# Performance work log

Hardware: AMD Instinct MI355X
Metric: run time of the kernel (lower is better)

The kernel has to match this reference:

```python
import jax, jax.numpy as jnp
import numpy as np

NUM_PRIMARY_CAPS = 8
PRIMARY_DIM = 8
NUM_CLASSES = 10
OUT_DIM = 16
CHANNELS = 32
NUM_ROUTING = 3
IN_UNITS1 = CHANNELS * 20 * 20  # 12800


def squash(s):
    # squash as written in the source: |s| / (1 + |s|^2) * s
    n = jnp.linalg.norm(s, axis=-1, keepdims=True)
    return n / (1.0 + n * n) * s


def routing(u_hat, num_routing):
    # u_hat: [B, num_caps, in_units, dim_caps]
    b = jnp.zeros(u_hat.shape[:3] + (1,), dtype=u_hat.dtype)
    v = None
    for it in range(num_routing):
        c = jax.nn.softmax(b, axis=1)                       # over num_caps
        s = jnp.sum(c * u_hat, axis=2, keepdims=True)        # [B,J,1,M]
        v = squash(s)
        if it < num_routing - 1:
            b = b + jnp.sum(u_hat * v, axis=-1, keepdims=True)
    return v[:, :, 0, :]                                     # [B, num_caps, dim_caps]


def setup_inputs() -> dict:
    key = jax.random.key(0)
    k1, k2, k3, k4, k5 = jax.random.split(key, 5)
    x = jax.random.normal(k1, (64, 1, 28, 28), dtype=jnp.float32)
    conv_w = jax.random.normal(k2, (CHANNELS, 1, 9, 9), dtype=jnp.float32) * 0.05
    conv_b = jax.random.normal(k3, (CHANNELS,), dtype=jnp.float32) * 0.05
    # W: [num_capsules, in_units, dim_capsules, in_channels]
    W1 = jax.random.normal(k4, (NUM_PRIMARY_CAPS, IN_UNITS1, PRIMARY_DIM, CHANNELS), dtype=jnp.float32) * 0.05
    W2 = jax.random.normal(k5, (NUM_CLASSES, NUM_PRIMARY_CAPS, OUT_DIM, PRIMARY_DIM), dtype=jnp.float32) * 0.05
    return {"x": x, "conv_w": conv_w, "conv_b": conv_b, "W1": W1, "W2": W2}


def reference(x, conv_w, conv_b, W1, W2):
    B = x.shape[0]
    # conv1 + relu: [B,1,28,28] -> [B,C,20,20]
    h = jax.lax.conv_general_dilated(
        x, conv_w, window_strides=(1, 1), padding='VALID',
        dimension_numbers=('NCHW', 'OIHW', 'NCHW'))
    h = jax.nn.relu(h + conv_b[None, :, None, None])
    # primary capsules: flatten features to in_units; the source einsum
    # 'ijkl,ijkm->ijkm' reduces W over its in_channels axis and broadcasts x,
    # so u_hat[b,j,k,m] = sum_c W1[j,k,m,c] * x[b,k]
    xf = h.reshape(B, IN_UNITS1)
    u1 = jnp.einsum('jkmc,bk->bjkm', W1, xf)   # [B, 8, 12800, primary_dim]
    v1 = routing(u1, 1)                         # [B, 8, primary_dim]
    # digit capsules: per-unit feature vectors, standard capsule transform
    u2 = jnp.einsum('jkmc,bkc->bjkm', W2, v1)   # [B, 10, 8, out_dim]
    v2 = routing(u2, NUM_ROUTING)               # [B, 10, out_dim]
    return v2
```

## Files before the change

kernel.cpp:

```cpp
#include <hip/hip_runtime.h>

typedef float f4 __attribute__((ext_vector_type(4)));

__device__ __forceinline__ float readlane_f(float v, int l) {
    return __int_as_float(__builtin_amdgcn_readlane(__float_as_int(v), l));
}

__global__ __launch_bounds__(256) void conv_kernel(
    const float* __restrict__ X, const float* __restrict__ CW, const float* __restrict__ CB,
    float* __restrict__ XT, float* __restrict__ S1acc)
{
    int blk = blockIdx.x;
    int b = blk >> 5, c = blk & 31;
    int t = threadIdx.x;
    if (blk < 16) S1acc[blk * 256 + t] = 0.0f;

    __shared__ float xs[784];
    const f4* xb4 = reinterpret_cast<const f4*>(X + b * 784);
    if (t < 196) {
        f4 v = xb4[t];
        float* d = &xs[t * 4];
        d[0] = v.x; d[1] = v.y; d[2] = v.z; d[3] = v.w;
    }
    __syncthreads();

    float bias = CB[c];
    const float* wcg = CW + c * 81;
    float w[81];
    #pragma unroll
    for (int i = 0; i < 81; ++i) w[i] = wcg[i];

    for (int p = t; p < 400; p += 256) {
        int py = p / 20, px = p - py * 20;
        float acc = bias;
        #pragma unroll
        for (int dy = 0; dy < 9; ++dy) {
            const float* xr = &xs[(py + dy) * 28 + px];
            #pragma unroll
            for (int dx = 0; dx < 9; ++dx)
                acc = fmaf(xr[dx], w[dy * 9 + dx], acc);
        }
        XT[(size_t)(c * 400 + p) * 64 + b] = acc > 0.f ? acc : 0.f;
    }
}

__global__ __launch_bounds__(256) void primary_kernel(
    const float* __restrict__ W1, const float* __restrict__ XT, float* __restrict__ S1acc)
{
    int kb = blockIdx.x;
    int j  = blockIdx.y;
    int t = threadIdx.x;
    int wave = t >> 6, lane = t & 63;
    int k0 = kb * 64 + wave * 16;
    const f4* Wp = reinterpret_cast<const f4*>(W1) + (size_t)j * 819200
                   + (size_t)k0 * 64 + lane;
    const float* Xp = XT + (size_t)k0 * 64 + lane;

    float acc[8] = {0.f,0.f,0.f,0.f,0.f,0.f,0.f,0.f};
    #pragma unroll 8
    for (int kk = 0; kk < 16; ++kk) {
        f4 w = __builtin_nontemporal_load(Wp); Wp += 64;
        float xv = *Xp; Xp += 64;
        float s = (w.x + w.y) + (w.z + w.w);
        s += __shfl_xor(s, 1);
        s += __shfl_xor(s, 2);
        s += __shfl_xor(s, 4);
        #pragma unroll
        for (int m = 0; m < 8; ++m)
            acc[m] = fmaf(xv, readlane_f(s, m * 8), acc[m]);
    }

    __shared__ float red[4][64][9];
    #pragma unroll
    for (int m = 0; m < 8; ++m) red[wave][lane][m] = acc[m];
    __syncthreads();
    for (int idx = t; idx < 512; idx += 256) {
        int bb = idx >> 3, m = idx & 7;
        float v = red[0][bb][m] + red[1][bb][m] + red[2][bb][m] + red[3][bb][m];
        atomicAdd(&S1acc[(bb * 8 + j) * 8 + m], v);
    }
}

__global__ __launch_bounds__(256) void routing_kernel(
    const float* __restrict__ W2, const float* __restrict__ S1acc,
    float* __restrict__ OUT)
{
    int b = blockIdx.x;
    int t = threadIdx.x;
    __shared__ float v1[64];
    __shared__ float u2[10][8][16];
    __shared__ float blog[10][8];
    __shared__ float cw[10][8];
    __shared__ float sv[10][16];
    __shared__ float vv[10][16];
    __shared__ float fac[16];

    if (t < 64) v1[t] = S1acc[b * 64 + t] * 0.125f;
    if (t >= 64 && t < 144) { int q = t - 64; blog[q >> 3][q & 7] = 0.f; }
    __syncthreads();
    if (t < 8) {
        float n2 = 0.f;
        #pragma unroll
        for (int m = 0; m < 8; ++m) { float x = v1[t * 8 + m]; n2 = fmaf(x, x, n2); }
        float n = sqrtf(n2);
        fac[t] = n / (1.f + n2);
    }
    __syncthreads();
    if (t < 64) v1[t] *= fac[t >> 3];
    __syncthreads();

    for (int idx = t; idx < 1280; idx += 256) {
        int j = idx >> 7;
        int r = idx & 127;
        int k = r >> 4, m = r & 15;
        const float* wp = W2 + idx * 8;
        float a = 0.f;
        #pragma unroll
        for (int c = 0; c < 8; ++c) a = fmaf(wp[c], v1[k * 8 + c], a);
        u2[j][k][m] = a;
    }
    __syncthreads();

    for (int it = 0; it < 3; ++it) {
        if (t < 8) {
            float mx = -1e30f;
            #pragma unroll
            for (int j = 0; j < 10; ++j) mx = fmaxf(mx, blog[j][t]);
            float e[10], se = 0.f;
            #pragma unroll
            for (int j = 0; j < 10; ++j) { e[j] = expf(blog[j][t] - mx); se += e[j]; }
            float inv = 1.f / se;
            #pragma unroll
            for (int j = 0; j < 10; ++j) cw[j][t] = e[j] * inv;
        }
        __syncthreads();
        if (t < 160) {
            int j = t >> 4, m = t & 15;
            float a = 0.f;
            #pragma unroll
            for (int k = 0; k < 8; ++k) a = fmaf(cw[j][k], u2[j][k][m], a);
            sv[j][m] = a;
        }
        __syncthreads();
        if (t < 10) {
            float n2 = 0.f;
            #pragma unroll
            for (int m = 0; m < 16; ++m) { float x = sv[t][m]; n2 = fmaf(x, x, n2); }
            float n = sqrtf(n2);
            fac[t] = n / (1.f + n2);
        }
        __syncthreads();
        if (t < 160) { int j = t >> 4, m = t & 15; vv[j][m] = sv[j][m] * fac[j]; }
        __syncthreads();
        if (it < 2) {
            if (t < 80) {
                int j = t >> 3, k = t & 7;
                float d = 0.f;
                #pragma unroll
                for (int m = 0; m < 16; ++m) d = fmaf(u2[j][k][m], vv[j][m], d);
                blog[j][k] += d;
            }
            __syncthreads();
        }
    }
    if (t < 160) OUT[b * 160 + t] = vv[t >> 4][t & 15];
}

extern "C" void kernel_launch(void* const* d_in, const int* in_sizes, int n_in,
                              void* d_out, int out_size, void* d_ws, size_t ws_size,
                              hipStream_t stream) {
    const float* X  = (const float*)d_in[0];
    const float* CW = (const float*)d_in[1];
    const float* CB = (const float*)d_in[2];
    const float* W1 = (const float*)d_in[3];
    const float* W2 = (const float*)d_in[4];
    float* S1 = (float*)d_ws;
    float* XT = (float*)((char*)d_ws + 16384);
    float* OUT = (float*)d_out;

    conv_kernel<<<2048, 256, 0, stream>>>(X, CW, CB, XT, S1);
    primary_kernel<<<dim3(200, 8), 256, 0, stream>>>(W1, XT, S1);
    routing_kernel<<<64, 256, 0, stream>>>(W2, S1, OUT);
}
```

Before: 172.7 us.

## Batch conv across images per block for coalesced stores; enlarge primary blocks

The conv kernel now runs one block per (row-pair, channel) and handles all 64 images, so each thread owns one image and writes to the batch-innermost XT layout with coalesced stores instead of strided single-float writes. Input rows for all images are staged in padded shared memory (about 72KB), which may limit occupancy. The primary kernel doubles its block to 512 threads covering 128 input units, halving the number of atomic adds into the accumulator.

```diff
diff --git a/kernel.cpp b/kernel.cpp
--- a/kernel.cpp
+++ b/kernel.cpp
@@ -10,17 +10,26 @@
     const float* __restrict__ X, const float* __restrict__ CW, const float* __restrict__ CB,
     float* __restrict__ XT, float* __restrict__ S1acc)
 {
-    int blk = blockIdx.x;
-    int b = blk >> 5, c = blk & 31;
-    int t = threadIdx.x;
-    if (blk < 16) S1acc[blk * 256 + t] = 0.0f;
+    int pb = blockIdx.x;
+    int c  = blockIdx.y;
+    int t  = threadIdx.x;
+    int bid = blockIdx.y * 10 + blockIdx.x;
+    if (bid < 16) S1acc[bid * 256 + t] = 0.0f;
 
-    __shared__ float xs[784];
-    const f4* xb4 = reinterpret_cast<const f4*>(X + b * 784);
-    if (t < 196) {
-        f4 v = xb4[t];
-        float* d = &xs[t * 4];
-        d[0] = v.x; d[1] = v.y; d[2] = v.z; d[3] = v.w;
+    __shared__ float xs[64][281];
+    int py0 = pb * 2;
+    {
+        int b = t >> 2, q = t & 3;
+        const f4* src = reinterpret_cast<const f4*>(X + b * 784 + py0 * 28);
+        #pragma unroll
+        for (int i = 0; i < 18; ++i) {
+            int idx4 = q + 4 * i;
+            if (idx4 < 70) {
+                f4 v = src[idx4];
+                float* d = &xs[b][idx4 * 4];
+                d[0] = v.x; d[1] = v.y; d[2] = v.z; d[3] = v.w;
+            }
+        }
     }
     __syncthreads();
 
@@ -30,28 +39,33 @@
     #pragma unroll
     for (int i = 0; i < 81; ++i) w[i] = wcg[i];
 
-    for (int p = t; p < 400; p += 256) {
+    int psub = t >> 6, b = t & 63;
+    size_t base = (size_t)(c * 400 + pb * 40) * 64;
+    #pragma unroll
+    for (int i = 0; i < 10; ++i) {
+        int p  = pb * 40 + i * 4 + psub;
         int py = p / 20, px = p - py * 20;
+        int pyr = py - py0;
         float acc = bias;
         #pragma unroll
         for (int dy = 0; dy < 9; ++dy) {
-            const float* xr = &xs[(py + dy) * 28 + px];
+            const float* xr = &xs[b][(pyr + dy) * 28 + px];
             #pragma unroll
             for (int dx = 0; dx < 9; ++dx)
                 acc = fmaf(xr[dx], w[dy * 9 + dx], acc);
         }
-        XT[(size_t)(c * 400 + p) * 64 + b] = acc > 0.f ? acc : 0.f;
+        XT[base + (size_t)i * 256 + (size_t)psub * 64 + b] = acc > 0.f ? acc : 0.f;
     }
 }
 
-__global__ __launch_bounds__(256) void primary_kernel(
+__global__ __launch_bounds__(512) void primary_kernel(
     const float* __restrict__ W1, const float* __restrict__ XT, float* __restrict__ S1acc)
 {
     int kb = blockIdx.x;
     int j  = blockIdx.y;
     int t = threadIdx.x;
     int wave = t >> 6, lane = t & 63;
-    int k0 = kb * 64 + wave * 16;
+    int k0 = kb * 128 + wave * 16;
     const f4* Wp = reinterpret_cast<const f4*>(W1) + (size_t)j * 819200
                    + (size_t)k0 * 64 + lane;
     const float* Xp = XT + (size_t)k0 * 64 + lane;
@@ -70,13 +84,14 @@
             acc[m] = fmaf(xv, readlane_f(s, m * 8), acc[m]);
     }
 
-    __shared__ float red[4][64][9];
+    __shared__ float red[8][64][9];
     #pragma unroll
     for (int m = 0; m < 8; ++m) red[wave][lane][m] = acc[m];
     __syncthreads();
-    for (int idx = t; idx < 512; idx += 256) {
-        int bb = idx >> 3, m = idx & 7;
-        float v = red[0][bb][m] + red[1][bb][m] + red[2][bb][m] + red[3][bb][m];
+    {
+        int bb = t >> 3, m = t & 7;
+        float v = red[0][bb][m] + red[1][bb][m] + red[2][bb][m] + red[3][bb][m]
+                + red[4][bb][m] + red[5][bb][m] + red[6][bb][m] + red[7][bb][m];
         atomicAdd(&S1acc[(bb * 8 + j) * 8 + m], v);
     }
 }
@@ -178,7 +193,7 @@
     float* XT = (float*)((char*)d_ws + 16384);
     float* OUT = (float*)d_out;
 
-    conv_kernel<<<2048, 256, 0, stream>>>(X, CW, CB, XT, S1);
-    primary_kernel<<<dim3(200, 8), 256, 0, stream>>>(W1, XT, S1);
+    conv_kernel<<<dim3(10, 32), 256, 0, stream>>>(X, CW, CB, XT, S1);
+    primary_kernel<<<dim3(100, 8), 512, 0, stream>>>(W1, XT, S1);
     routing_kernel<<<64, 256, 0, stream>>>(W2, S1, OUT);
 }
```

Measured after the change: 173.9 us. Within noise of the previous version (+0.7%).

## Fuse conv into primary capsule kernel and replace atomics with partial-sum buffer

Applied to the files above, without the earlier changes.

Merges the convolution and primary-capsule reduction into one kernel. Each block computes a 50-position slice of one conv channel for all 64 batches into shared memory, then 8 waves (one per primary capsule) stream the matching W1 rows. Per-block partial sums go to a workspace buffer and the routing kernel reduces them, so the XT round trip, the zeroing and the global atomics all disappear. The cost is a grid of only 256 blocks of 512 threads for streaming roughly 105MB of W1, which may limit memory-level parallelism compared with the earlier 1600-block launch.

```diff
diff --git a/kernel.cpp b/kernel.cpp
--- a/kernel.cpp
+++ b/kernel.cpp
@@ -6,62 +6,68 @@
     return __int_as_float(__builtin_amdgcn_readlane(__float_as_int(v), l));
 }
 
-__global__ __launch_bounds__(256) void conv_kernel(
+__global__ __launch_bounds__(512) void fused_kernel(
     const float* __restrict__ X, const float* __restrict__ CW, const float* __restrict__ CB,
-    float* __restrict__ XT, float* __restrict__ S1acc)
+    const float* __restrict__ W1, float* __restrict__ S1P)
 {
-    int blk = blockIdx.x;
-    int b = blk >> 5, c = blk & 31;
+    int i = blockIdx.x;
+    int c = i >> 3, p0 = (i & 7) * 50;
     int t = threadIdx.x;
-    if (blk < 16) S1acc[blk * 256 + t] = 0.0f;
+    int wave = t >> 6, lane = t & 63;
 
-    __shared__ float xs[784];
-    const f4* xb4 = reinterpret_cast<const f4*>(X + b * 784);
-    if (t < 196) {
-        f4 v = xb4[t];
-        float* d = &xs[t * 4];
-        d[0] = v.x; d[1] = v.y; d[2] = v.z; d[3] = v.w;
-    }
-    __syncthreads();
+    __shared__ float xs[32][309];
+    __shared__ float xt[50][64];
+
+    int py0 = p0 / 20;
 
     float bias = CB[c];
     const float* wcg = CW + c * 81;
     float w[81];
     #pragma unroll
-    for (int i = 0; i < 81; ++i) w[i] = wcg[i];
+    for (int q = 0; q < 81; ++q) w[q] = wcg[q];
 
-    for (int p = t; p < 400; p += 256) {
-        int py = p / 20, px = p - py * 20;
-        float acc = bias;
-        #pragma unroll
-        for (int dy = 0; dy < 9; ++dy) {
-            const float* xr = &xs[(py + dy) * 28 + px];
+    for (int h = 0; h < 2; ++h) {
+        {
+            int b = t >> 4, q = t & 15;
+            const f4* src = reinterpret_cast<const f4*>(X + (size_t)(b + 32 * h) * 784 + py0 * 28);
             #pragma unroll
-            for (int dx = 0; dx < 9; ++dx)
-                acc = fmaf(xr[dx], w[dy * 9 + dx], acc);
+            for (int it2 = 0; it2 < 5; ++it2) {
+                int idx4 = q + 16 * it2;
+                if (idx4 < 77) {
+                    f4 v = src[idx4];
+                    float* d = &xs[b][idx4 * 4];
+                    d[0] = v.x; d[1] = v.y; d[2] = v.z; d[3] = v.w;
+                }
+            }
         }
-        XT[(size_t)(c * 400 + p) * 64 + b] = acc > 0.f ? acc : 0.f;
+        __syncthreads();
+        {
+            int psub = t >> 5, b = t & 31;
+            for (int pl = psub; pl < 50; pl += 16) {
+                int p = p0 + pl;
+                int py = p / 20, px = p - py * 20;
+                const float* xrow = &xs[b][(py - py0) * 28 + px];
+                float acc = bias;
+                #pragma unroll
+                for (int dy = 0; dy < 9; ++dy)
+                    #pragma unroll
+                    for (int dx = 0; dx < 9; ++dx)
+                        acc = fmaf(xrow[dy * 28 + dx], w[dy * 9 + dx], acc);
+                xt[pl][b + 32 * h] = acc > 0.f ? acc : 0.f;
+            }
+        }
+        __syncthreads();
     }
-}
 
-__global__ __launch_bounds__(256) void primary_kernel(
-    const float* __restrict__ W1, const float* __restrict__ XT, float* __restrict__ S1acc)
-{
-    int kb = blockIdx.x;
-    int j  = blockIdx.y;
-    int t = threadIdx.x;
-    int wave = t >> 6, lane = t & 63;
-    int k0 = kb * 64 + wave * 16;
-    const f4* Wp = reinterpret_cast<const f4*>(W1) + (size_t)j * 819200
+    int k0 = c * 400 + p0;
+    const f4* Wp = reinterpret_cast<const f4*>(W1) + (size_t)wave * 819200
                    + (size_t)k0 * 64 + lane;
-    const float* Xp = XT + (size_t)k0 * 64 + lane;
-
     float acc[8] = {0.f,0.f,0.f,0.f,0.f,0.f,0.f,0.f};
-    #pragma unroll 8
-    for (int kk = 0; kk < 16; ++kk) {
-        f4 w = __builtin_nontemporal_load(Wp); Wp += 64;
-        float xv = *Xp; Xp += 64;
-        float s = (w.x + w.y) + (w.z + w.w);
+    #pragma unroll 10
+    for (int kk = 0; kk < 50; ++kk) {
+        f4 wv = __builtin_nontemporal_load(Wp); Wp += 64;
+        float xv = xt[kk][lane];
+        float s = (wv.x + wv.y) + (wv.z + wv.w);
         s += __shfl_xor(s, 1);
         s += __shfl_xor(s, 2);
         s += __shfl_xor(s, 4);
@@ -70,23 +76,20 @@
             acc[m] = fmaf(xv, readlane_f(s, m * 8), acc[m]);
     }
 
-    __shared__ float red[4][64][9];
-    #pragma unroll
-    for (int m = 0; m < 8; ++m) red[wave][lane][m] = acc[m];
-    __syncthreads();
-    for (int idx = t; idx < 512; idx += 256) {
-        int bb = idx >> 3, m = idx & 7;
-        float v = red[0][bb][m] + red[1][bb][m] + red[2][bb][m] + red[3][bb][m];
-        atomicAdd(&S1acc[(bb * 8 + j) * 8 + m], v);
-    }
+    float* dst = S1P + ((((size_t)i * 8 + wave) * 64 + lane) * 8);
+    f4 lo = {acc[0], acc[1], acc[2], acc[3]};
+    f4 hi = {acc[4], acc[5], acc[6], acc[7]};
+    reinterpret_cast<f4*>(dst)[0] = lo;
+    reinterpret_cast<f4*>(dst)[1] = hi;
 }
 
 __global__ __launch_bounds__(256) void routing_kernel(
-    const float* __restrict__ W2, const float* __restrict__ S1acc,
+    const float* __restrict__ W2, const float* __restrict__ S1P,
     float* __restrict__ OUT)
 {
     int b = blockIdx.x;
     int t = threadIdx.x;
+    __shared__ float part[64][4];
     __shared__ float v1[64];
     __shared__ float u2[10][8][16];
     __shared__ float blog[10][8];
@@ -95,7 +98,18 @@
     __shared__ float vv[10][16];
     __shared__ float fac[16];
 
-    if (t < 64) v1[t] = S1acc[b * 64 + t] * 0.125f;
+    {
+        int jm = t >> 2, r = t & 3;
+        int j = jm >> 3, m = jm & 7;
+        size_t base = (size_t)j * 512 + (size_t)b * 8 + m;
+        float ssum = 0.f;
+        #pragma unroll 16
+        for (int ii = r; ii < 256; ii += 4)
+            ssum += S1P[base + (size_t)ii * 4096];
+        part[jm][r] = ssum;
+    }
+    __syncthreads();
+    if (t < 64) v1[t] = (part[t][0] + part[t][1] + part[t][2] + part[t][3]) * 0.125f;
     if (t >= 64 && t < 144) { int q = t - 64; blog[q >> 3][q & 7] = 0.f; }
     __syncthreads();
     if (t < 8) {
@@ -116,7 +130,7 @@
         const float* wp = W2 + idx * 8;
         float a = 0.f;
         #pragma unroll
-        for (int c = 0; c < 8; ++c) a = fmaf(wp[c], v1[k * 8 + c], a);
+        for (int cc = 0; cc < 8; ++cc) a = fmaf(wp[cc], v1[k * 8 + cc], a);
         u2[j][k][m] = a;
     }
     __syncthreads();
@@ -174,11 +188,9 @@
     const float* CB = (const float*)d_in[2];
     const float* W1 = (const float*)d_in[3];
     const float* W2 = (const float*)d_in[4];
-    float* S1 = (float*)d_ws;
-    float* XT = (float*)((char*)d_ws + 16384);
+    float* S1P = (float*)d_ws;
     float* OUT = (float*)d_out;
 
-    conv_kernel<<<2048, 256, 0, stream>>>(X, CW, CB, XT, S1);
-    primary_kernel<<<dim3(200, 8), 256, 0, stream>>>(W1, XT, S1);
-    routing_kernel<<<64, 256, 0, stream>>>(W2, S1, OUT);
+    fused_kernel<<<256, 512, 0, stream>>>(X, CW, CB, W1, S1P);
+    routing_kernel<<<64, 256, 0, stream>>>(W2, S1P, OUT);
 }
```

Measured after the change: 168.6 us. 1.02x faster.
